# Kernel tuning notes

Hardware: AMD Instinct MI355X
Metric: run time of the kernel (lower is better)

Reference implementation:

```python
import jax, jax.numpy as jnp
import numpy as np

D_MODEL = 1024
N_HEADS = 16
HEAD_DIM = D_MODEL // N_HEADS
D_FF = 4096
EPS = 1e-5


def _layer_norm(x, gamma, beta):
    mu = jnp.mean(x, axis=-1, keepdims=True)
    var = jnp.var(x, axis=-1, keepdims=True)
    return (x - mu) * jax.lax.rsqrt(var + EPS) * gamma + beta


def setup_inputs() -> dict:
    key = jax.random.key(0)
    ks = jax.random.split(key, 16)
    B, T, S = 2, 2048, 2048
    s = 1.0 / np.sqrt(D_MODEL)
    inp = {
        "tgt": jax.random.normal(ks[0], (B, T, D_MODEL), jnp.float32),
        "memory": jax.random.normal(ks[1], (B, S, D_MODEL), jnp.float32),
        "wq": jax.random.normal(ks[2], (D_MODEL, D_MODEL), jnp.float32) * s,
        "bq": jnp.zeros((D_MODEL,), jnp.float32),
        "wk": jax.random.normal(ks[3], (D_MODEL, D_MODEL), jnp.float32) * s,
        "bk": jnp.zeros((D_MODEL,), jnp.float32),
        "wv": jax.random.normal(ks[4], (D_MODEL, D_MODEL), jnp.float32) * s,
        "bv": jnp.zeros((D_MODEL,), jnp.float32),
        "wo": jax.random.normal(ks[5], (D_MODEL, D_MODEL), jnp.float32) * s,
        "bo": jnp.zeros((D_MODEL,), jnp.float32),
        "w1": jax.random.normal(ks[6], (D_MODEL, D_FF), jnp.float32) * s,
        "b1": jnp.zeros((D_FF,), jnp.float32),
        "w2": jax.random.normal(ks[7], (D_FF, D_MODEL), jnp.float32) * (1.0 / np.sqrt(D_FF)),
        "b2": jnp.zeros((D_MODEL,), jnp.float32),
        "g1": jnp.ones((D_MODEL,), jnp.float32),
        "be1": jnp.zeros((D_MODEL,), jnp.float32),
        "g2": jnp.ones((D_MODEL,), jnp.float32),
        "be2": jnp.zeros((D_MODEL,), jnp.float32),
    }
    return inp


def reference(tgt, memory, wq, bq, wk, bk, wv, bv, wo, bo, w1, b1, w2, b2, g1, be1, g2, be2):
    B, T, _ = tgt.shape
    S = memory.shape[1]
    scale = HEAD_DIM ** -0.5
    # projections -> [B, H, L, Dh]
    Q = (tgt @ wq + bq).reshape(B, T, N_HEADS, HEAD_DIM).transpose(0, 2, 1, 3)
    K = (memory @ wk + bk).reshape(B, S, N_HEADS, HEAD_DIM).transpose(0, 2, 1, 3)
    V = (memory @ wv + bv).reshape(B, S, N_HEADS, HEAD_DIM).transpose(0, 2, 1, 3)
    scores = jnp.einsum("bhtd,bhsd->bhts", Q, K) * scale
    attn = jax.nn.softmax(scores, axis=-1)  # dropout=0 (eval)
    ctx = jnp.einsum("bhts,bhsd->bhtd", attn, V)
    ctx = ctx.transpose(0, 2, 1, 3).reshape(B, T, D_MODEL)
    attn_out = ctx @ wo + bo
    # post-norm residual blocks
    x = _layer_norm(tgt + attn_out, g1, be1)
    ff = jax.nn.relu(x @ w1 + b1) @ w2 + b2
    out = _layer_norm(x + ff, g2, be2)
    return out
```

## Files before the change

### kernel.cpp

```cpp
#include <hip/hip_runtime.h>


typedef unsigned short u16;
typedef __attribute__((ext_vector_type(8))) short bvec8;
typedef __attribute__((ext_vector_type(4))) float fvec4;
typedef __attribute__((ext_vector_type(4))) unsigned uvec4;

#define MFMA16(a, b, c) __builtin_amdgcn_mfma_f32_16x16x32_bf16((a), (b), (c), 0, 0, 0)

__device__ __forceinline__ u16 f2b(float f) {
  union { float f; unsigned u; } x; x.f = f;
  unsigned u = x.u;
  return (u16)((u + 0x7FFFu + ((u >> 16) & 1u)) >> 16);
}
__device__ __forceinline__ unsigned cvtpk(float lo, float hi) {
  unsigned r;
  asm("v_cvt_pk_bf16_f32 %0, %1, %2" : "=v"(r) : "v"(lo), "v"(hi));
  return r;
}
#define PLSWAP32(a, b) asm("v_permlane32_swap_b32 %0, %1" : "+v"(a), "+v"(b))
#define PLSWAP16(a, b) asm("v_permlane16_swap_b32 %0, %1" : "+v"(a), "+v"(b))

__device__ __forceinline__ void gl_lds16(const u16* g, u16* lds) {
  __builtin_amdgcn_global_load_lds(
      (const __attribute__((address_space(1))) void*)g,
      (__attribute__((address_space(3))) void*)lds, 16, 0, 0);
}

__global__ __launch_bounds__(256) void k_pre(
    const float* __restrict__ tgt, const float* __restrict__ mem,
    const float* __restrict__ wq, const float* __restrict__ wk,
    const float* __restrict__ wv, const float* __restrict__ wo,
    const float* __restrict__ w1, const float* __restrict__ w2,
    u16* __restrict__ tgt_b, u16* __restrict__ mem_b,
    u16* __restrict__ wqT, u16* __restrict__ wkvT, u16* __restrict__ woT,
    u16* __restrict__ w1T, u16* __restrict__ w2T) {
  __shared__ float t[32][33];
  int bb = blockIdx.x;
  if (bb < 8192) {
    const float* in = (bb < 4096) ? tgt : mem;
    u16* outp = (bb < 4096) ? tgt_b : mem_b;
    int i = (bb & 4095) * 256 + threadIdx.x;
    float4 v = ((const float4*)in)[i];
    ushort4 o;
    o.x = f2b(v.x); o.y = f2b(v.y); o.z = f2b(v.z); o.w = f2b(v.w);
    ((ushort4*)outp)[i] = o;
    return;
  }
  int b = bb - 8192;
  const float* W; u16* WT; int K, N, bx, by;
  if (b < 4096) {
    int m = b >> 10, tt = b & 1023;
    bx = tt & 31; by = tt >> 5; K = 1024; N = 1024;
    W = (m == 0) ? wq : (m == 1) ? wk : (m == 2) ? wv : wo;
    WT = (m == 0) ? wqT : (m == 1) ? wkvT : (m == 2) ? wkvT + 1024 * 1024 : woT;
  } else if (b < 8192) {
    int tt = b - 4096; bx = tt & 127; by = tt >> 7; K = 1024; N = 4096;
    W = w1; WT = w1T;
  } else {
    int tt = b - 8192; bx = tt & 31; by = tt >> 5; K = 4096; N = 1024;
    W = w2; WT = w2T;
  }
  int tx = threadIdx.x & 31, ty = threadIdx.x >> 5;
  int n0 = bx * 32, k0 = by * 32;
#pragma unroll
  for (int i = 0; i < 4; i++)
    t[ty + i * 8][tx] = W[(size_t)(k0 + ty + i * 8) * N + n0 + tx];
  __syncthreads();
#pragma unroll
  for (int i = 0; i < 4; i++)
    WT[(size_t)(n0 + ty + i * 8) * K + k0 + tx] = f2b(t[tx][ty + i * 8]);
}

__global__ __launch_bounds__(256, 4) void k_qkv(
    const u16* __restrict__ tgt_b, const u16* __restrict__ mem_b,
    const u16* __restrict__ wqT, const u16* __restrict__ wkvT,
    const float* __restrict__ bq, const float* __restrict__ bk,
    const float* __restrict__ bv,
    u16* __restrict__ Qb, u16* __restrict__ Kb, u16* __restrict__ Vtb) {
  __shared__ u16 S[256 * 64];
  const int tid = threadIdx.x, w = tid >> 6, lane = tid & 63;
  const int q = lane >> 4, l = lane & 15;
  const bool isQ = blockIdx.x < 256;
  const int pq = isQ ? blockIdx.x : blockIdx.x - 256;
  const int lx = (pq >> 3) & (isQ ? 7 : 15);
  const int ly = (pq & 7) + ((pq >> (isQ ? 6 : 7)) << 3);
  const int m0 = ly * 128, n0 = lx * 128;
  const u16* A = isQ ? tgt_b : mem_b;
  const u16* BT = isQ ? wqT : wkvT;
  const int wm = (w >> 1) * 64, wn = (w & 1) * 64;
  const int rowin = lane >> 3, grp = lane & 7;
  const int gcol = ((grp + rowin) & 7) * 8;
  const int kc0 = ((q + 8 - (l & 7)) & 7) * 8;
  const int kc1 = ((q + 12 - (l & 7)) & 7) * 8;
  const u16* gp[8];
  u16* lp[8];
#pragma unroll
  for (int c = 0; c < 8; c++) {
    int r0 = (w * 8 + c) * 8;
    gp[c] = (r0 < 128) ? A + (size_t)(m0 + r0 + rowin) * 1024 + gcol
                       : BT + (size_t)(n0 + r0 - 128 + rowin) * 1024 + gcol;
    lp[c] = &S[r0 * 64];
  }
  fvec4 acc[4][4] = {};
#pragma unroll 1
  for (int k0 = 0; k0 < 1024; k0 += 64) {
#pragma unroll
    for (int c = 0; c < 8; c++) gl_lds16(gp[c] + k0, lp[c]);
    __syncthreads();
#pragma unroll
    for (int kh = 0; kh < 2; kh++) {
      const int kc = kh ? kc1 : kc0;
      bvec8 af[4], bf[4];
#pragma unroll
      for (int i = 0; i < 4; i++) {
        af[i] = *(const bvec8*)&S[(wm + 16 * i + l) * 64 + kc];
        bf[i] = *(const bvec8*)&S[(128 + wn + 16 * i + l) * 64 + kc];
      }
#pragma unroll
      for (int i = 0; i < 4; i++)
#pragma unroll
        for (int j = 0; j < 4; j++)
          acc[i][j] = MFMA16(af[i], bf[j], acc[i][j]);
    }
    __syncthreads();
  }
#pragma unroll
  for (int mi = 0; mi < 4; mi++)
#pragma unroll
    for (int ni = 0; ni < 4; ni++) {
      int row = m0 + wm + mi * 16 + q * 4;
      int col = n0 + wn + ni * 16 + l;
      if (isQ) {
        float bvv = bq[col];
#pragma unroll
        for (int r = 0; r < 4; r++)
          Qb[(size_t)(row + r) * 1024 + col] = f2b((acc[mi][ni][r] + bvv) * 0.125f);
      } else if (col < 1024) {
        float bvv = bk[col];
#pragma unroll
        for (int r = 0; r < 4; r++)
          Kb[(size_t)(row + r) * 1024 + col] = f2b(acc[mi][ni][r] + bvv);
      } else {
        int vcol = col - 1024;
        float bvv = bv[vcol];
        int b = row >> 11, s = row & 2047;
        int h = vcol >> 6, d = vcol & 63;
        ushort4 o;
        o.x = f2b(acc[mi][ni][0] + bvv);
        o.y = f2b(acc[mi][ni][1] + bvv);
        o.z = f2b(acc[mi][ni][2] + bvv);
        o.w = f2b(acc[mi][ni][3] + bvv);
        *(ushort4*)&Vtb[((size_t)(b * 16 + h) * 64 + d) * 2048 + s] = o;
      }
    }
}

template <int TM, int TN>
__global__ __launch_bounds__(256, 4) void k_gemm(
    const u16* __restrict__ A, const u16* __restrict__ BT,
    const float* __restrict__ bias, const float* __restrict__ resid,
    float* __restrict__ outF, u16* __restrict__ outB,
    int M, int N, int Kstride, int Klen, float scale, int flags) {
  constexpr int WM = TM / 2, WN = TN / 2;
  constexpr int MI = WM / 16, NI = WN / 16;
  constexpr int NCALL = (TM + TN) / 32;
  __shared__ u16 S[(TM + TN) * 64];
  const int tid = threadIdx.x, w = tid >> 6, lane = tid & 63;
  const int q = lane >> 4, l = lane & 15;
  const int nx = gridDim.x, nyh = gridDim.y >> 3;
  const int p = blockIdx.x + nx * (blockIdx.y + gridDim.y * blockIdx.z);
  const int q8 = p >> 3;
  const int lx = q8 & (nx - 1);
  const int t = q8 >> __builtin_ctz(nx);
  const int ly = (p & 7) + ((t & (nyh - 1)) << 3);
  const int lz = t >> __builtin_ctz(nyh);
  const int m0 = ly * TM, n0 = lx * TN;
  const int kbeg = lz * Klen;
  const int wm = (w >> 1) * WM, wn = (w & 1) * WN;
  const int rowin = lane >> 3, grp = lane & 7;
  const int gcol = ((grp + rowin) & 7) * 8;
  const int kc0 = ((q + 8 - (l & 7)) & 7) * 8;
  const int kc1 = ((q + 12 - (l & 7)) & 7) * 8;
  const u16* gp[NCALL];
  u16* lp[NCALL];
#pragma unroll
  for (int c = 0; c < NCALL; c++) {
    int r0 = (w * NCALL + c) * 8;
    gp[c] = (r0 < TM) ? A + (size_t)(m0 + r0 + rowin) * Kstride + kbeg + gcol
                      : BT + (size_t)(n0 + r0 - TM + rowin) * Kstride + kbeg + gcol;
    lp[c] = &S[r0 * 64];
  }
  fvec4 acc[MI][NI] = {};
#pragma unroll 1
  for (int k0 = 0; k0 < Klen; k0 += 64) {
#pragma unroll
    for (int c = 0; c < NCALL; c++) gl_lds16(gp[c] + k0, lp[c]);
    __syncthreads();
#pragma unroll
    for (int kh = 0; kh < 2; kh++) {
      const int kc = kh ? kc1 : kc0;
      bvec8 af[MI], bf[NI];
#pragma unroll
      for (int i = 0; i < MI; i++)
        af[i] = *(const bvec8*)&S[(wm + 16 * i + l) * 64 + kc];
#pragma unroll
      for (int j = 0; j < NI; j++)
        bf[j] = *(const bvec8*)&S[(TM + wn + 16 * j + l) * 64 + kc];
#pragma unroll
      for (int i = 0; i < MI; i++)
#pragma unroll
        for (int j = 0; j < NI; j++)
          acc[i][j] = MFMA16(af[i], bf[j], acc[i][j]);
    }
    __syncthreads();
  }
  if (flags & 16) {
    float* po = outF + (size_t)lz * M * N;
#pragma unroll
    for (int mi = 0; mi < MI; mi++)
#pragma unroll
      for (int ni = 0; ni < NI; ni++) {
        int row = m0 + wm + mi * 16 + q * 4;
        int col = n0 + wn + ni * 16 + l;
#pragma unroll
        for (int r = 0; r < 4; r++)
          po[(size_t)(row + r) * N + col] = acc[mi][ni][r];
      }
    return;
  }
#pragma unroll
  for (int mi = 0; mi < MI; mi++)
#pragma unroll
    for (int ni = 0; ni < NI; ni++) {
      int row = m0 + wm + mi * 16 + q * 4;
      int col = n0 + wn + ni * 16 + l;
      float bvv = bias[col];
#pragma unroll
      for (int r = 0; r < 4; r++) {
        float v = (acc[mi][ni][r] + bvv) * scale;
        if (flags & 1) v = fmaxf(v, 0.0f);
        size_t idx = (size_t)(row + r) * N + col;
        if (flags & 8) v += resid[idx];
        if (flags & 2) outB[idx] = f2b(v);
        if (flags & 4) outF[idx] = v;
      }
    }
}

__global__ __launch_bounds__(256, 4) void k_attn(
    const u16* __restrict__ Q, const u16* __restrict__ Kb,
    const u16* __restrict__ Vt, float* __restrict__ opart,
    float* __restrict__ lpart) {
  __shared__ u16 Ks[2][64 * 64];
  __shared__ u16 Vs[2][64 * 64];
  const int tid = threadIdx.x, w = tid >> 6, lane = tid & 63;
  const int q = lane >> 4, l = lane & 15;
  const int bx = blockIdx.x;
  const int blk = (bx & 7) * 64 + (bx >> 3);
  const int bh = blk >> 4, tb = blk & 15;
  const int b = bh >> 4, h = bh & 15;
  const int t0 = tb * 128 + w * 32;
  const int sbeg = blockIdx.y * 1024;
  float* op = opart + (size_t)blockIdx.y * 4096 * 1024;
  float* lp = lpart + (size_t)blockIdx.y * 4096 * 16;
  const u16* Qp = Q + (size_t)(b * 2048 + t0) * 1024 + h * 64;
  const u16* Kp = Kb + (size_t)(b * 2048) * 1024 + h * 64;
  const u16* Vp = Vt + (size_t)bh * 64 * 2048;
  const int rowin = lane >> 3, grp = lane & 7;
  const int gcol = ((grp + rowin) & 7) * 8;
  const int kc0 = ((q + 8 - (l & 7)) & 7) * 8;
  const int kc1 = ((q + 12 - (l & 7)) & 7) * 8;
  bvec8 aQ[2][2];
#pragma unroll
  for (int ti = 0; ti < 2; ti++)
#pragma unroll
    for (int kh = 0; kh < 2; kh++)
      aQ[ti][kh] = *(const bvec8*)&Qp[(size_t)(ti * 16 + l) * 1024 + kh * 32 + q * 8];
  fvec4 o[2][4] = {};
  float ls[2] = {0.f, 0.f};
  auto stage = [&](int bb, int sv) {
    gl_lds16(Kp + (size_t)(sv + w * 8 + rowin) * 1024 + gcol, &Ks[bb][(w * 8) * 64]);
    gl_lds16(Kp + (size_t)(sv + 32 + w * 8 + rowin) * 1024 + gcol, &Ks[bb][(32 + w * 8) * 64]);
    gl_lds16(Vp + (size_t)(w * 8 + rowin) * 2048 + sv + gcol, &Vs[bb][(w * 8) * 64]);
    gl_lds16(Vp + (size_t)(32 + w * 8 + rowin) * 2048 + sv + gcol, &Vs[bb][(32 + w * 8) * 64]);
  };
  stage(0, sbeg);
  int cur = 0;
#pragma unroll 1
  for (int s0 = sbeg; s0 < sbeg + 1024; s0 += 64) {
    __syncthreads();
    if (s0 + 64 < sbeg + 1024) stage(cur ^ 1, s0 + 64);
    const u16* KsC = Ks[cur];
    const u16* VsC = Vs[cur];
    unsigned pw[2][4][2];
    __builtin_amdgcn_s_setprio(1);
#pragma unroll
    for (int ss = 0; ss < 4; ss++) {
      const int ro = (ss * 16 + l) * 64;
      bvec8 kf0 = *(const bvec8*)&KsC[ro + kc0];
      bvec8 kf1 = *(const bvec8*)&KsC[ro + kc1];
#pragma unroll
      for (int ti = 0; ti < 2; ti++) {
        fvec4 sc = {0.f, 0.f, 0.f, 0.f};
        sc = MFMA16(kf0, aQ[ti][0], sc);
        sc = MFMA16(kf1, aQ[ti][1], sc);
        float p0 = __expf(sc[0]), p1 = __expf(sc[1]);
        float p2 = __expf(sc[2]), p3 = __expf(sc[3]);
        ls[ti] += (p0 + p1) + (p2 + p3);
        pw[ti][ss][0] = cvtpk(p0, p1);
        pw[ti][ss][1] = cvtpk(p2, p3);
      }
    }
    __builtin_amdgcn_s_setprio(0);
#pragma unroll
    for (int ti = 0; ti < 2; ti++)
#pragma unroll
      for (int b4 = 0; b4 < 2; b4++)
#pragma unroll
        for (int r2 = 0; r2 < 2; r2++) {
          PLSWAP32(pw[ti][2 * b4][r2], pw[ti][2 * b4 + 1][r2]);
          PLSWAP16(pw[ti][2 * b4][r2], pw[ti][2 * b4 + 1][r2]);
        }
    bvec8 bP[2][2];
#pragma unroll
    for (int ti = 0; ti < 2; ti++)
#pragma unroll
      for (int kh = 0; kh < 2; kh++) {
        uvec4 t = {pw[ti][2 * kh][0], pw[ti][2 * kh][1],
                   pw[ti][2 * kh + 1][0], pw[ti][2 * kh + 1][1]};
        bP[ti][kh] = __builtin_bit_cast(bvec8, t);
      }
    bvec8 bV[4][2];
#pragma unroll
    for (int dt = 0; dt < 4; dt++) {
      const int ro = (dt * 16 + l) * 64;
      bV[dt][0] = *(const bvec8*)&VsC[ro + kc0];
      bV[dt][1] = *(const bvec8*)&VsC[ro + kc1];
    }
    __builtin_amdgcn_s_setprio(1);
#pragma unroll
    for (int dt = 0; dt < 4; dt++)
#pragma unroll
      for (int ti = 0; ti < 2; ti++) {
        o[ti][dt] = MFMA16(bV[dt][0], bP[ti][0], o[ti][dt]);
        o[ti][dt] = MFMA16(bV[dt][1], bP[ti][1], o[ti][dt]);
      }
    __builtin_amdgcn_s_setprio(0);
    cur ^= 1;
  }
#pragma unroll
  for (int ti = 0; ti < 2; ti++) {
    float s = ls[ti];
    s += __shfl_xor(s, 16, 64);
    s += __shfl_xor(s, 32, 64);
    int trow = b * 2048 + t0 + ti * 16 + l;
    if (q == 0) lp[trow * 16 + h] = s;
#pragma unroll
    for (int dt = 0; dt < 4; dt++)
      *(fvec4*)&op[(size_t)trow * 1024 + h * 64 + dt * 16 + q * 4] = o[ti][dt];
  }
}

__global__ __launch_bounds__(256) void k_actx(const float* __restrict__ opart,
                                              const float* __restrict__ lpart,
                                              u16* __restrict__ ctx) {
  int row = blockIdx.x, c0 = threadIdx.x * 4;
  int h = c0 >> 6;
  float lsum = lpart[row * 16 + h] + lpart[4096 * 16 + row * 16 + h];
  float inv = 1.0f / lsum;
  float4 a = *(const float4*)&opart[(size_t)row * 1024 + c0];
  float4 b = *(const float4*)&opart[(size_t)4096 * 1024 + (size_t)row * 1024 + c0];
  ushort4 o;
  o.x = f2b((a.x + b.x) * inv);
  o.y = f2b((a.y + b.y) * inv);
  o.z = f2b((a.z + b.z) * inv);
  o.w = f2b((a.w + b.w) * inv);
  *(ushort4*)&ctx[(size_t)row * 1024 + c0] = o;
}

__global__ __launch_bounds__(256) void k_lnp(
    const float* __restrict__ parts, int nparts,
    const float* __restrict__ bias, const float* __restrict__ resid,
    const float* __restrict__ g, const float* __restrict__ be,
    float* __restrict__ xf, u16* __restrict__ xb) {
  __shared__ float sm[8];
  int row = blockIdx.x, tid = threadIdx.x;
  size_t base = (size_t)row * 1024;
  const size_t pstride = (size_t)4096 * 1024;
  float v[4], s = 0.f, ss = 0.f;
#pragma unroll
  for (int j = 0; j < 4; j++) {
    int c = tid + j * 256;
    float acc = bias[c] + resid[base + c];
    for (int z = 0; z < nparts; z++) acc += parts[z * pstride + base + c];
    v[j] = acc;
    s += acc; ss += acc * acc;
  }
#pragma unroll
  for (int off = 32; off; off >>= 1) {
    s += __shfl_down(s, off, 64);
    ss += __shfl_down(ss, off, 64);
  }
  int w = tid >> 6;
  if ((tid & 63) == 0) { sm[w] = s; sm[4 + w] = ss; }
  __syncthreads();
  float S = sm[0] + sm[1] + sm[2] + sm[3];
  float SS = sm[4] + sm[5] + sm[6] + sm[7];
  float mean = S * (1.0f / 1024.0f);
  float var = SS * (1.0f / 1024.0f) - mean * mean;
  float rstd = rsqrtf(var + 1e-5f);
#pragma unroll
  for (int j = 0; j < 4; j++) {
    int c = tid + j * 256;
    float o = (v[j] - mean) * rstd * g[c] + be[c];
    xf[base + c] = o;
    if (xb) xb[base + c] = f2b(o);
  }
}

extern "C" void kernel_launch(void* const* d_in, const int* in_sizes, int n_in,
                              void* d_out, int out_size, void* d_ws, size_t ws_size,
                              hipStream_t stream) {
  (void)in_sizes; (void)n_in; (void)out_size; (void)ws_size;
  const float* tgt = (const float*)d_in[0];
  const float* mem = (const float*)d_in[1];
  const float* wq  = (const float*)d_in[2];
  const float* bq  = (const float*)d_in[3];
  const float* wk  = (const float*)d_in[4];
  const float* bk  = (const float*)d_in[5];
  const float* wv  = (const float*)d_in[6];
  const float* bv  = (const float*)d_in[7];
  const float* wo  = (const float*)d_in[8];
  const float* bo  = (const float*)d_in[9];
  const float* w1  = (const float*)d_in[10];
  const float* b1  = (const float*)d_in[11];
  const float* w2  = (const float*)d_in[12];
  const float* b2  = (const float*)d_in[13];
  const float* g1  = (const float*)d_in[14];
  const float* be1 = (const float*)d_in[15];
  const float* g2  = (const float*)d_in[16];
  const float* be2 = (const float*)d_in[17];
  float* out = (float*)d_out;

  char* ws = (char*)d_ws;
  size_t off = 0;
  auto take = [&](size_t bytes) { char* p = ws + off; off += bytes; return p; };
  const size_t MB = 1024 * 1024;
  u16* tgt_b = (u16*)take(8 * MB);
  u16* mem_b = (u16*)take(8 * MB);
  u16* wqT   = (u16*)take(2 * MB);
  u16* wkvT  = (u16*)take(4 * MB);
  u16* woT   = (u16*)take(2 * MB);
  u16* w1T   = (u16*)take(8 * MB);
  u16* w2T   = (u16*)take(8 * MB);
  u16* Qb    = (u16*)take(8 * MB);
  u16* Kb    = (u16*)take(8 * MB);
  u16* Vtb   = (u16*)take(8 * MB);
  u16* ctx   = (u16*)take(8 * MB);
  float* opart = (float*)take(32 * MB);
  float* opj   = (float*)take(32 * MB);
  float* lpart = (float*)take(1 * MB);
  float* xf  = (float*)take(16 * MB);
  u16* xb    = (u16*)take(8 * MB);
  u16* hbuf  = Qb;
  float* fp2 = opart;

  k_pre<<<20480, 256, 0, stream>>>(tgt, mem, wq, wk, wv, wo, w1, w2,
                                   tgt_b, mem_b, wqT, wkvT, woT, w1T, w2T);
  k_qkv<<<768, 256, 0, stream>>>(tgt_b, mem_b, wqT, wkvT, bq, bk, bv,
                                 Qb, Kb, Vtb);
  k_attn<<<dim3(512, 2), 256, 0, stream>>>(Qb, Kb, Vtb, opart, lpart);
  k_actx<<<4096, 256, 0, stream>>>(opart, lpart, ctx);
  k_gemm<64, 128><<<dim3(8, 64, 1), 256, 0, stream>>>(
      ctx, woT, nullptr, nullptr, opj, nullptr,
      4096, 1024, 1024, 1024, 1.0f, 16);
  k_lnp<<<4096, 256, 0, stream>>>(opj, 1, bo, tgt, g1, be1, xf, xb);
  k_gemm<128, 128><<<dim3(32, 32), 256, 0, stream>>>(
      xb, w1T, b1, nullptr, nullptr, hbuf,
      4096, 4096, 1024, 1024, 1.0f, 1 | 2);
  k_gemm<64, 128><<<dim3(8, 64, 2), 256, 0, stream>>>(
      hbuf, w2T, nullptr, nullptr, fp2, nullptr,
      4096, 1024, 4096, 2048, 1.0f, 16);
  k_lnp<<<4096, 256, 0, stream>>>(fp2, 2, b2, xf, g2, be2, out, nullptr);
}
```

Baseline: 372.2 us.

## Double-buffer LDS tiles in QKV and GEMM kernels to overlap loads with MFMA

The QKV projection and generic GEMM kernels now use two LDS buffers. The next K-slice's global-to-LDS copy is issued right after the barrier, while the current slice is consumed by MFMAs, which removes the second barrier per iteration. LDS use doubles, so launch-bounds occupancy hints drop to 2 or 3 blocks per SM. That trades occupancy for latency hiding. Correctness depends on the single barrier ordering the async LDS writes against reads of the other buffer.

```diff
diff --git a/kernel.cpp b/kernel.cpp
--- a/kernel.cpp
+++ b/kernel.cpp
@@ -72,13 +72,13 @@
     WT[(size_t)(n0 + ty + i * 8) * K + k0 + tx] = f2b(t[tx][ty + i * 8]);
 }
 
-__global__ __launch_bounds__(256, 4) void k_qkv(
+__global__ __launch_bounds__(256, 2) void k_qkv(
     const u16* __restrict__ tgt_b, const u16* __restrict__ mem_b,
     const u16* __restrict__ wqT, const u16* __restrict__ wkvT,
     const float* __restrict__ bq, const float* __restrict__ bk,
     const float* __restrict__ bv,
     u16* __restrict__ Qb, u16* __restrict__ Kb, u16* __restrict__ Vtb) {
-  __shared__ u16 S[256 * 64];
+  __shared__ u16 S[2][256 * 64];
   const int tid = threadIdx.x, w = tid >> 6, lane = tid & 63;
   const int q = lane >> 4, l = lane & 15;
   const bool isQ = blockIdx.x < 256;
@@ -94,28 +94,34 @@
   const int kc0 = ((q + 8 - (l & 7)) & 7) * 8;
   const int kc1 = ((q + 12 - (l & 7)) & 7) * 8;
   const u16* gp[8];
-  u16* lp[8];
+  int lpo[8];
 #pragma unroll
   for (int c = 0; c < 8; c++) {
     int r0 = (w * 8 + c) * 8;
     gp[c] = (r0 < 128) ? A + (size_t)(m0 + r0 + rowin) * 1024 + gcol
                        : BT + (size_t)(n0 + r0 - 128 + rowin) * 1024 + gcol;
-    lp[c] = &S[r0 * 64];
-  }
+    lpo[c] = r0 * 64;
+  }
+  auto stage = [&](int bb, int k0) {
+#pragma unroll
+    for (int c = 0; c < 8; c++) gl_lds16(gp[c] + k0, &S[bb][lpo[c]]);
+  };
   fvec4 acc[4][4] = {};
+  stage(0, 0);
+  int cur = 0;
 #pragma unroll 1
   for (int k0 = 0; k0 < 1024; k0 += 64) {
-#pragma unroll
-    for (int c = 0; c < 8; c++) gl_lds16(gp[c] + k0, lp[c]);
     __syncthreads();
+    if (k0 + 64 < 1024) stage(cur ^ 1, k0 + 64);
+    const u16* SC = S[cur];
 #pragma unroll
     for (int kh = 0; kh < 2; kh++) {
       const int kc = kh ? kc1 : kc0;
       bvec8 af[4], bf[4];
 #pragma unroll
       for (int i = 0; i < 4; i++) {
-        af[i] = *(const bvec8*)&S[(wm + 16 * i + l) * 64 + kc];
-        bf[i] = *(const bvec8*)&S[(128 + wn + 16 * i + l) * 64 + kc];
+        af[i] = *(const bvec8*)&SC[(wm + 16 * i + l) * 64 + kc];
+        bf[i] = *(const bvec8*)&SC[(128 + wn + 16 * i + l) * 64 + kc];
       }
 #pragma unroll
       for (int i = 0; i < 4; i++)
@@ -123,7 +129,7 @@
         for (int j = 0; j < 4; j++)
           acc[i][j] = MFMA16(af[i], bf[j], acc[i][j]);
     }
-    __syncthreads();
+    cur ^= 1;
   }
 #pragma unroll
   for (int mi = 0; mi < 4; mi++)
@@ -156,8 +162,8 @@
     }
 }
 
-template <int TM, int TN>
-__global__ __launch_bounds__(256, 4) void k_gemm(
+template <int TM, int TN, int MINW>
+__global__ __launch_bounds__(256, MINW) void k_gemm(
     const u16* __restrict__ A, const u16* __restrict__ BT,
     const float* __restrict__ bias, const float* __restrict__ resid,
     float* __restrict__ outF, u16* __restrict__ outB,
@@ -165,7 +171,7 @@
   constexpr int WM = TM / 2, WN = TN / 2;
   constexpr int MI = WM / 16, NI = WN / 16;
   constexpr int NCALL = (TM + TN) / 32;
-  __shared__ u16 S[(TM + TN) * 64];
+  __shared__ u16 S[2][(TM + TN) * 64];
   const int tid = threadIdx.x, w = tid >> 6, lane = tid & 63;
   const int q = lane >> 4, l = lane & 15;
   const int nx = gridDim.x, nyh = gridDim.y >> 3;
@@ -183,37 +189,43 @@
   const int kc0 = ((q + 8 - (l & 7)) & 7) * 8;
   const int kc1 = ((q + 12 - (l & 7)) & 7) * 8;
   const u16* gp[NCALL];
-  u16* lp[NCALL];
+  int lpo[NCALL];
 #pragma unroll
   for (int c = 0; c < NCALL; c++) {
     int r0 = (w * NCALL + c) * 8;
     gp[c] = (r0 < TM) ? A + (size_t)(m0 + r0 + rowin) * Kstride + kbeg + gcol
                       : BT + (size_t)(n0 + r0 - TM + rowin) * Kstride + kbeg + gcol;
-    lp[c] = &S[r0 * 64];
-  }
+    lpo[c] = r0 * 64;
+  }
+  auto stage = [&](int bb, int k0) {
+#pragma unroll
+    for (int c = 0; c < NCALL; c++) gl_lds16(gp[c] + k0, &S[bb][lpo[c]]);
+  };
   fvec4 acc[MI][NI] = {};
+  stage(0, 0);
+  int cur = 0;
 #pragma unroll 1
   for (int k0 = 0; k0 < Klen; k0 += 64) {
-#pragma unroll
-    for (int c = 0; c < NCALL; c++) gl_lds16(gp[c] + k0, lp[c]);
     __syncthreads();
+    if (k0 + 64 < Klen) stage(cur ^ 1, k0 + 64);
+    const u16* SC = S[cur];
 #pragma unroll
     for (int kh = 0; kh < 2; kh++) {
       const int kc = kh ? kc1 : kc0;
       bvec8 af[MI], bf[NI];
 #pragma unroll
       for (int i = 0; i < MI; i++)
-        af[i] = *(const bvec8*)&S[(wm + 16 * i + l) * 64 + kc];
+        af[i] = *(const bvec8*)&SC[(wm + 16 * i + l) * 64 + kc];
 #pragma unroll
       for (int j = 0; j < NI; j++)
-        bf[j] = *(const bvec8*)&S[(TM + wn + 16 * j + l) * 64 + kc];
+        bf[j] = *(const bvec8*)&SC[(TM + wn + 16 * j + l) * 64 + kc];
 #pragma unroll
       for (int i = 0; i < MI; i++)
 #pragma unroll
         for (int j = 0; j < NI; j++)
           acc[i][j] = MFMA16(af[i], bf[j], acc[i][j]);
     }
-    __syncthreads();
+    cur ^= 1;
   }
   if (flags & 16) {
     float* po = outF + (size_t)lz * M * N;
@@ -472,14 +484,14 @@
                                  Qb, Kb, Vtb);
   k_attn<<<dim3(512, 2), 256, 0, stream>>>(Qb, Kb, Vtb, opart, lpart);
   k_actx<<<4096, 256, 0, stream>>>(opart, lpart, ctx);
-  k_gemm<64, 128><<<dim3(8, 64, 1), 256, 0, stream>>>(
+  k_gemm<64, 128, 3><<<dim3(8, 64, 1), 256, 0, stream>>>(
       ctx, woT, nullptr, nullptr, opj, nullptr,
       4096, 1024, 1024, 1024, 1.0f, 16);
   k_lnp<<<4096, 256, 0, stream>>>(opj, 1, bo, tgt, g1, be1, xf, xb);
-  k_gemm<128, 128><<<dim3(32, 32), 256, 0, stream>>>(
+  k_gemm<128, 128, 2><<<dim3(32, 32), 256, 0, stream>>>(
       xb, w1T, b1, nullptr, nullptr, hbuf,
       4096, 4096, 1024, 1024, 1.0f, 1 | 2);
-  k_gemm<64, 128><<<dim3(8, 64, 2), 256, 0, stream>>>(
+  k_gemm<64, 128, 3><<<dim3(8, 64, 2), 256, 0, stream>>>(
       hbuf, w2T, nullptr, nullptr, fp2, nullptr,
       4096, 1024, 4096, 2048, 1.0f, 16);
   k_lnp<<<4096, 256, 0, stream>>>(fp2, 2, b2, xf, g2, be2, out, nullptr);
```

After: 384.6 us. +3.3%, slower.
